# Kernel tuning notes

Measured on AMD Instinct MI355X. Metric: run time of the kernel, lower is better.

## Reference

```python
import jax, jax.numpy as jnp
import numpy as np

NEG_SLOPE = 0.2  # PyG GATConv default leaky_relu slope


def gat_conv(x, src, dst, n, W, a_src, a_dst, bias, concat):
    """PyG-style GATConv (add_self_loops already applied to src/dst)."""
    H, C = a_src.shape
    h = (x @ W).reshape(n, H, C)                      # [N,H,C]
    al_src = jnp.einsum('nhc,hc->nh', h, a_src)       # [N,H]
    al_dst = jnp.einsum('nhc,hc->nh', h, a_dst)       # [N,H]
    e = jax.nn.leaky_relu(al_src[src] + al_dst[dst], NEG_SLOPE)  # [E,H]
    # segment softmax over incoming edges of each dst node
    m = jax.ops.segment_max(e, dst, num_segments=n)   # [N,H]
    ex = jnp.exp(e - m[dst])
    denom = jax.ops.segment_sum(ex, dst, num_segments=n)
    alpha = ex / denom[dst]                            # [E,H]
    out = jax.ops.segment_sum(h[src] * alpha[:, :, None], dst, num_segments=n)  # [N,H,C]
    if concat:
        out = out.reshape(n, H * C)
    else:
        out = out.mean(axis=1)
    return out + bias


def setup_inputs() -> dict:
    key = jax.random.key(0)
    ks = jax.random.split(key, 12)
    N, E = 100000, 1600000
    IN, HID, OUT, H = 128, 16, 32, 4
    x = jax.random.normal(ks[0], (N, IN), dtype=jnp.float32)
    edge_index = jax.random.randint(ks[1], (2, E), 0, N, dtype=jnp.int64)
    s = 0.1
    W1 = jax.random.normal(ks[2], (IN, H * HID), dtype=jnp.float32) * s
    a_src1 = jax.random.normal(ks[3], (H, HID), dtype=jnp.float32) * s
    a_dst1 = jax.random.normal(ks[4], (H, HID), dtype=jnp.float32) * s
    b1 = jnp.zeros((H * HID,), dtype=jnp.float32)
    W2 = jax.random.normal(ks[5], (H * HID, H * OUT), dtype=jnp.float32) * s
    a_src2 = jax.random.normal(ks[6], (H, OUT), dtype=jnp.float32) * s
    a_dst2 = jax.random.normal(ks[7], (H, OUT), dtype=jnp.float32) * s
    b2 = jnp.zeros((OUT,), dtype=jnp.float32)
    return {"x": x, "edge_index": edge_index,
            "W1": W1, "a_src1": a_src1, "a_dst1": a_dst1, "b1": b1,
            "W2": W2, "a_src2": a_src2, "a_dst2": a_dst2, "b2": b2}


def reference(x, edge_index, W1, a_src1, a_dst1, b1, W2, a_src2, a_dst2, b2):
    n = x.shape[0]
    loop = jnp.arange(n, dtype=edge_index.dtype)
    src = jnp.concatenate([edge_index[0], loop])
    dst = jnp.concatenate([edge_index[1], loop])
    # dropout is identity at inference
    h = gat_conv(x, src, dst, n, W1, a_src1, a_dst1, b1, concat=True)
    h = gat_conv(h, src, dst, n, W2, a_src2, a_dst2, b2, concat=False)
    h = jax.nn.elu(h)
    return jax.nn.log_softmax(h, axis=1)
```

## Files before the change

kernel.cpp:

```cpp
#include <hip/hip_runtime.h>
#include <hip/hip_fp16.h>
#include <cstdint>
#include <cstddef>

#define NEG 0.2f
#define TILE 4096
#define WEXP(e) __expf((e) > 0.f ? (e) : NEG * (e))


__global__ __launch_bounds__(256) void bhist_k(const int* __restrict__ ei, int* __restrict__ bc, int E, int nbk) {
    __shared__ int sb[256];
    int t = threadIdx.x;
    sb[t] = 0;
    __syncthreads();
    int stride = gridDim.x * 256;
    for (int i = blockIdx.x * 256 + t; i < E; i += stride) {
        int d = __builtin_nontemporal_load(ei + E + i);
        atomicAdd(&sb[d >> 9], 1);
    }
    __syncthreads();
    if (t < nbk && sb[t] > 0) atomicAdd(&bc[t], sb[t]);
}


__global__ __launch_bounds__(256) void bscan_k(const int* __restrict__ bc, int* __restrict__ bb,
                                               int* __restrict__ curA, int nbk) {
    __shared__ int sm[256];
    int t = threadIdx.x;
    int v = (t < nbk) ? bc[t] : 0;
    sm[t] = v; __syncthreads();
    for (int off = 1; off < 256; off <<= 1) {
        int u = (t >= off) ? sm[t - off] : 0;
        __syncthreads();
        sm[t] += u;
        __syncthreads();
    }
    if (t < nbk) {
        int ex = sm[t] - v;
        bb[t] = ex;
        curA[t] = ex;
        if (t == nbk - 1) bb[nbk] = sm[t];
    }
}


__global__ __launch_bounds__(256) void partA_k(const int* __restrict__ ei, int* __restrict__ curA,
                                               uint2* __restrict__ pairs, int E, int nbk) {
    __shared__ int scnt[256];
    __shared__ int sc[256];
    __shared__ int sbase[256];
    __shared__ int gbase[256];
    __shared__ int cur2[256];
    __shared__ int ssrc[TILE];
    __shared__ int sdst[TILE];
    int t = threadIdx.x;
    int ntiles = (E + TILE - 1) / TILE;
    for (int tile = blockIdx.x; tile < ntiles; tile += gridDim.x) {
        int base = tile * TILE;
        int cntE = min(TILE, E - base);
        scnt[t] = 0;
        __syncthreads();
        int mys[16], myd[16];
        #pragma unroll
        for (int j = 0; j < 16; j++) {
            int i = base + t + 256 * j;
            int s = 0, d = -1;
            if (i < E) {
                s = __builtin_nontemporal_load(ei + i);
                d = __builtin_nontemporal_load(ei + E + i);
            }
            mys[j] = s; myd[j] = d;
            if (d >= 0) atomicAdd(&scnt[d >> 9], 1);
        }
        __syncthreads();
        sc[t] = scnt[t];
        __syncthreads();
        for (int off = 1; off < 256; off <<= 1) {
            int u = (t >= off) ? sc[t - off] : 0;
            __syncthreads();
            sc[t] += u;
            __syncthreads();
        }
        int myb = sc[t] - scnt[t];
        sbase[t] = myb;
        cur2[t] = myb;
        if (t < nbk && scnt[t] > 0) gbase[t] = atomicAdd(&curA[t], scnt[t]);
        __syncthreads();
        #pragma unroll
        for (int j = 0; j < 16; j++) {
            int d = myd[j];
            if (d >= 0) {
                int b = d >> 9;
                int pos = atomicAdd(&cur2[b], 1);
                ssrc[pos] = mys[j];
                sdst[pos] = d;
            }
        }
        __syncthreads();
        for (int i = t; i < cntE; i += 256) {
            int d = sdst[i];
            int b = d >> 9;
            int addr = gbase[b] + (i - sbase[b]);
            pairs[addr] = make_uint2((unsigned)ssrc[i], (unsigned)d);
        }
        __syncthreads();
    }
}


__global__ __launch_bounds__(256) void partB2_k(const uint2* __restrict__ pin, const int* __restrict__ bb,
                                                int* __restrict__ rp, int* __restrict__ cnt,
                                                int* __restrict__ srcout, int N) {
    __shared__ int cur[512];
    __shared__ int sc[512];
    int b = blockIdx.x, t = threadIdx.x;
    int d0 = b << 9;
    cur[t] = 0; cur[t + 256] = 0;
    __syncthreads();
    int ebase = bb[b], eend = bb[b + 1];
    for (int j = ebase + t; j < eend; j += 256) {
        int d = (int)pin[j].y;
        atomicAdd(&cur[d - d0], 1);
    }
    __syncthreads();
    sc[t] = cur[t]; sc[t + 256] = cur[t + 256];
    __syncthreads();
    for (int off = 1; off <= 256; off <<= 1) {
        int a0 = (t >= off) ? sc[t - off] : 0;
        int a1 = sc[t + 256 - off];
        __syncthreads();
        sc[t] += a0; sc[t + 256] += a1;
        __syncthreads();
    }
    int base0 = ebase + sc[t] - cur[t];
    int base1 = ebase + sc[t + 256] - cur[t + 256];
    if (d0 + t < N)       { rp[d0 + t] = base0;       cnt[d0 + t] = cur[t]; }
    if (d0 + t + 256 < N) { rp[d0 + t + 256] = base1; cnt[d0 + t + 256] = cur[t + 256]; }
    cur[t] = base0; cur[t + 256] = base1;
    __syncthreads();
    for (int j = ebase + t; j < eend; j += 256) {
        uint2 p = pin[j];
        int d = (int)p.y;
        int pos = atomicAdd(&cur[d - d0], 1);
        srcout[pos] = (int)p.x;
    }
}


__global__ __launch_bounds__(256) void gemm1_k(const float* __restrict__ x, const float* __restrict__ W,
                                               const float* __restrict__ a_src, const float* __restrict__ a_dst,
                                               __half* __restrict__ h, float* __restrict__ alsrc,
                                               float* __restrict__ aldst, int N) {
    __shared__ float Bs[128 * 64];
    __shared__ float xs[64][68];
    int t = threadIdx.x;
    for (int i = t; i < 128 * 64 / 4; i += 256)
        ((float4*)Bs)[i] = ((const float4*)W)[i];
    int ct = t & 15, rt = t >> 4;
    int head = ct >> 2, cq = ct & 3;
    float asv[4], adv[4];
    #pragma unroll
    for (int j = 0; j < 4; j++) {
        asv[j] = a_src[head * 16 + 4 * cq + j];
        adv[j] = a_dst[head * 16 + 4 * cq + j];
    }
    int ntiles = (N + 63) >> 6;
    for (int tile = blockIdx.x; tile < ntiles; tile += gridDim.x) {
        int r0 = tile << 6;
        float acc[4][4];
        #pragma unroll
        for (int i = 0; i < 4; i++)
            #pragma unroll
            for (int j = 0; j < 4; j++) acc[i][j] = 0.f;
        for (int kc = 0; kc < 128; kc += 64) {
            __syncthreads();
            int srow = t >> 4, sf4 = t & 15;
            #pragma unroll
            for (int p = 0; p < 4; p++) {
                int r = r0 + srow + 16 * p;
                float4 v = make_float4(0.f, 0.f, 0.f, 0.f);
                if (r < N) v = *(const float4*)(x + (size_t)r * 128 + kc + 4 * sf4);
                *(float4*)&xs[srow + 16 * p][4 * sf4] = v;
            }
            __syncthreads();
            #pragma unroll 4
            for (int k = 0; k < 64; k++) {
                float4 bv = *(float4*)&Bs[(kc + k) * 64 + 4 * ct];
                #pragma unroll
                for (int i = 0; i < 4; i++) {
                    float xv = xs[4 * rt + i][k];
                    acc[i][0] = fmaf(xv, bv.x, acc[i][0]);
                    acc[i][1] = fmaf(xv, bv.y, acc[i][1]);
                    acc[i][2] = fmaf(xv, bv.z, acc[i][2]);
                    acc[i][3] = fmaf(xv, bv.w, acc[i][3]);
                }
            }
        }
        #pragma unroll
        for (int i = 0; i < 4; i++) {
            int r = r0 + 4 * rt + i;
            float ps = 0.f, pd = 0.f;
            #pragma unroll
            for (int j = 0; j < 4; j++) {
                ps = fmaf(acc[i][j], asv[j], ps);
                pd = fmaf(acc[i][j], adv[j], pd);
            }
            ps += __shfl_xor(ps, 1); ps += __shfl_xor(ps, 2);
            pd += __shfl_xor(pd, 1); pd += __shfl_xor(pd, 2);
            if (r < N) {
                __half2 h0 = __floats2half2_rn(acc[i][0], acc[i][1]);
                __half2 h1 = __floats2half2_rn(acc[i][2], acc[i][3]);
                *(__half2*)(h + (size_t)r * 64 + 4 * ct) = h0;
                *(__half2*)(h + (size_t)r * 64 + 4 * ct + 2) = h1;
                if (cq == 0) { alsrc[r * 4 + head] = ps; aldst[r * 4 + head] = pd; }
            }
        }
    }
}


__global__ __launch_bounds__(256) void node1_k(const __half* __restrict__ h, const int* __restrict__ srccol,
                                               const float* __restrict__ alsrc, const float* __restrict__ aldst,
                                               const int* __restrict__ rp, const int* __restrict__ cnt,
                                               const float* __restrict__ bias, __half* __restrict__ out, int N) {
    int t = threadIdx.x;
    int d = (blockIdx.x * 256 + t) >> 4;
    if (d >= N) return;
    int c = t & 15;
    int hc = c >> 2;
    const __half2* hb = (const __half2*)h;
    unsigned co = 2u * c;
    float ad = aldst[d * 4 + hc];
    float e = alsrc[d * 4 + hc] + ad;
    float w = WEXP(e);
    float den = w;
    __half2 wp = __float2half2_rn(w);
    uint2 u = *(const uint2*)(hb + ((unsigned)d << 5) + co);
    __half2 acc0 = __hmul2(wp, *(__half2*)&u.x);
    __half2 acc1 = __hmul2(wp, *(__half2*)&u.y);
    int start = rp[d], deg = cnt[d];
    int i = 0;
    for (; i + 3 < deg; i += 4) {
        int s0 = srccol[start + i];
        int s1 = srccol[start + i + 1];
        int s2 = srccol[start + i + 2];
        int s3 = srccol[start + i + 3];
        uint2 u0 = *(const uint2*)(hb + ((unsigned)s0 << 5) + co);
        uint2 u1 = *(const uint2*)(hb + ((unsigned)s1 << 5) + co);
        uint2 u2 = *(const uint2*)(hb + ((unsigned)s2 << 5) + co);
        uint2 u3 = *(const uint2*)(hb + ((unsigned)s3 << 5) + co);
        float e0 = alsrc[s0 * 4 + hc] + ad;
        float e1 = alsrc[s1 * 4 + hc] + ad;
        float e2 = alsrc[s2 * 4 + hc] + ad;
        float e3 = alsrc[s3 * 4 + hc] + ad;
        float w0 = WEXP(e0);
        float w1 = WEXP(e1);
        float w2 = WEXP(e2);
        float w3 = WEXP(e3);
        den += (w0 + w1) + (w2 + w3);
        __half2 p0 = __float2half2_rn(w0), p1 = __float2half2_rn(w1);
        __half2 p2 = __float2half2_rn(w2), p3 = __float2half2_rn(w3);
        acc0 = __hfma2(p0, *(__half2*)&u0.x, acc0);
        acc1 = __hfma2(p0, *(__half2*)&u0.y, acc1);
        acc0 = __hfma2(p1, *(__half2*)&u1.x, acc0);
        acc1 = __hfma2(p1, *(__half2*)&u1.y, acc1);
        acc0 = __hfma2(p2, *(__half2*)&u2.x, acc0);
        acc1 = __hfma2(p2, *(__half2*)&u2.y, acc1);
        acc0 = __hfma2(p3, *(__half2*)&u3.x, acc0);
        acc1 = __hfma2(p3, *(__half2*)&u3.y, acc1);
    }
    for (; i < deg; i++) {
        int s = srccol[start + i];
        uint2 us = *(const uint2*)(hb + ((unsigned)s << 5) + co);
        float es = alsrc[s * 4 + hc] + ad;
        float ws = WEXP(es);
        den += ws;
        __half2 wps = __float2half2_rn(ws);
        acc0 = __hfma2(wps, *(__half2*)&us.x, acc0);
        acc1 = __hfma2(wps, *(__half2*)&us.y, acc1);
    }
    float inv = 1.f / den;
    float2 f0 = __half22float2(acc0), f1 = __half22float2(acc1);
    float4 b = *(const float4*)(bias + 4 * c);
    __half2 o0 = __floats2half2_rn(f0.x * inv + b.x, f0.y * inv + b.y);
    __half2 o1 = __floats2half2_rn(f1.x * inv + b.z, f1.y * inv + b.w);
    uint2 o; o.x = *(unsigned*)&o0; o.y = *(unsigned*)&o1;
    *(uint2*)(out + (size_t)d * 64 + 4 * c) = o;
}


__global__ __launch_bounds__(256) void prew_k(const float* __restrict__ W2, const float* __restrict__ as2,
                                              const float* __restrict__ ad2, float* __restrict__ was,
                                              float* __restrict__ wad) {
    int t = threadIdx.x;
    int k = t >> 2, hh = t & 3;
    const float* wrow = W2 + k * 128 + hh * 32;
    const float* av = as2 + hh * 32;
    const float* dv = ad2 + hh * 32;
    float s = 0.f, ds = 0.f;
    #pragma unroll 8
    for (int c = 0; c < 32; c++) {
        float w = wrow[c];
        s = fmaf(w, av[c], s);
        ds = fmaf(w, dv[c], ds);
    }
    was[t] = s;
    wad[t] = ds;
}


__global__ __launch_bounds__(256) void alv2_k(const __half* __restrict__ h1o, const float* __restrict__ was,
                                              const float* __restrict__ wad, float* __restrict__ alsrc,
                                              float* __restrict__ aldst, int N) {
    int t = threadIdx.x;
    int d = (blockIdx.x * 256 + t) >> 4;
    if (d >= N) return;
    int c = t & 15;
    uint2 u = *(const uint2*)(h1o + (size_t)d * 64 + 4 * c);
    float2 f0 = __half22float2(*(__half2*)&u.x);
    float2 f1 = __half22float2(*(__half2*)&u.y);
    float v0 = f0.x, v1 = f0.y, v2 = f1.x, v3 = f1.y;
    const float4* was4 = (const float4*)was;
    const float4* wad4 = (const float4*)wad;
    float4 wa0 = was4[4 * c + 0], wa1 = was4[4 * c + 1], wa2 = was4[4 * c + 2], wa3 = was4[4 * c + 3];
    float4 wd0 = wad4[4 * c + 0], wd1 = wad4[4 * c + 1], wd2 = wad4[4 * c + 2], wd3 = wad4[4 * c + 3];
    float4 ps, pd;
    ps.x = fmaf(v0, wa0.x, fmaf(v1, wa1.x, fmaf(v2, wa2.x, v3 * wa3.x)));
    ps.y = fmaf(v0, wa0.y, fmaf(v1, wa1.y, fmaf(v2, wa2.y, v3 * wa3.y)));
    ps.z = fmaf(v0, wa0.z, fmaf(v1, wa1.z, fmaf(v2, wa2.z, v3 * wa3.z)));
    ps.w = fmaf(v0, wa0.w, fmaf(v1, wa1.w, fmaf(v2, wa2.w, v3 * wa3.w)));
    pd.x = fmaf(v0, wd0.x, fmaf(v1, wd1.x, fmaf(v2, wd2.x, v3 * wd3.x)));
    pd.y = fmaf(v0, wd0.y, fmaf(v1, wd1.y, fmaf(v2, wd2.y, v3 * wd3.y)));
    pd.z = fmaf(v0, wd0.z, fmaf(v1, wd1.z, fmaf(v2, wd2.z, v3 * wd3.z)));
    pd.w = fmaf(v0, wd0.w, fmaf(v1, wd1.w, fmaf(v2, wd2.w, v3 * wd3.w)));
    #pragma unroll
    for (int off = 1; off <= 8; off <<= 1) {
        ps.x += __shfl_xor(ps.x, off); ps.y += __shfl_xor(ps.y, off);
        ps.z += __shfl_xor(ps.z, off); ps.w += __shfl_xor(ps.w, off);
        pd.x += __shfl_xor(pd.x, off); pd.y += __shfl_xor(pd.y, off);
        pd.z += __shfl_xor(pd.z, off); pd.w += __shfl_xor(pd.w, off);
    }
    if (c == 0) {
        *(float4*)(alsrc + (size_t)d * 4) = ps;
        *(float4*)(aldst + (size_t)d * 4) = pd;
    }
}


#define EDGE2(U, F) { \
    float wa = WEXP(F.x + ad4.x), wb = WEXP(F.y + ad4.y); \
    float wc = WEXP(F.z + ad4.z), wd = WEXP(F.w + ad4.w); \
    dnA += wa; dnB += wb; dnC += wc; dnD += wd; \
    __half2 l = *(__half2*)&U.x, hh = *(__half2*)&U.y; \
    __half2 qa = __float2half2_rn(wa), qb = __float2half2_rn(wb); \
    __half2 qc = __float2half2_rn(wc), qd = __float2half2_rn(wd); \
    aA0 = __hfma2(qa, l, aA0); aA1 = __hfma2(qa, hh, aA1); \
    aB0 = __hfma2(qb, l, aB0); aB1 = __hfma2(qb, hh, aB1); \
    aC0 = __hfma2(qc, l, aC0); aC1 = __hfma2(qc, hh, aC1); \
    aD0 = __hfma2(qd, l, aD0); aD1 = __hfma2(qd, hh, aD1); }

__global__ __launch_bounds__(256) void node2_k(const __half* __restrict__ h1o, const int* __restrict__ srccol,
                                               const float* __restrict__ alsrc, const float* __restrict__ aldst,
                                               const int* __restrict__ rp, const int* __restrict__ cnt,
                                               __half* __restrict__ y, int N) {
    int t = threadIdx.x;
    int d = (blockIdx.x * 256 + t) >> 4;
    if (d >= N) return;
    int c = t & 15;
    const uint2* hb = (const uint2*)h1o;
    float4 ad4 = *(const float4*)(aldst + 4 * (size_t)d);
    float4 e4  = *(const float4*)(alsrc + 4 * (size_t)d);
    float wA = WEXP(e4.x + ad4.x);
    float wB = WEXP(e4.y + ad4.y);
    float wC = WEXP(e4.z + ad4.z);
    float wD = WEXP(e4.w + ad4.w);
    float dnA = wA, dnB = wB, dnC = wC, dnD = wD;
    uint2 u = hb[((size_t)d << 4) + c];
    __half2 lo = *(__half2*)&u.x, hi = *(__half2*)&u.y;
    __half2 pA = __float2half2_rn(wA), pB = __float2half2_rn(wB);
    __half2 pC = __float2half2_rn(wC), pD = __float2half2_rn(wD);
    __half2 aA0 = __hmul2(pA, lo), aA1 = __hmul2(pA, hi);
    __half2 aB0 = __hmul2(pB, lo), aB1 = __hmul2(pB, hi);
    __half2 aC0 = __hmul2(pC, lo), aC1 = __hmul2(pC, hi);
    __half2 aD0 = __hmul2(pD, lo), aD1 = __hmul2(pD, hi);
    int start = rp[d], deg = cnt[d];
    int i = 0;
    for (; i + 3 < deg; i += 4) {
        int s0 = srccol[start + i];
        int s1 = srccol[start + i + 1];
        int s2 = srccol[start + i + 2];
        int s3 = srccol[start + i + 3];
        uint2 u0 = hb[((size_t)s0 << 4) + c];
        uint2 u1 = hb[((size_t)s1 << 4) + c];
        uint2 u2 = hb[((size_t)s2 << 4) + c];
        uint2 u3 = hb[((size_t)s3 << 4) + c];
        float4 f0 = *(const float4*)(alsrc + 4 * (size_t)s0);
        float4 f1 = *(const float4*)(alsrc + 4 * (size_t)s1);
        float4 f2 = *(const float4*)(alsrc + 4 * (size_t)s2);
        float4 f3 = *(const float4*)(alsrc + 4 * (size_t)s3);
        EDGE2(u0, f0)
        EDGE2(u1, f1)
        EDGE2(u2, f2)
        EDGE2(u3, f3)
    }
    for (; i < deg; i++) {
        int s = srccol[start + i];
        uint2 us = hb[((size_t)s << 4) + c];
        float4 fs = *(const float4*)(alsrc + 4 * (size_t)s);
        EDGE2(us, fs)
    }
    float ivA = 0.25f / dnA, ivB = 0.25f / dnB, ivC = 0.25f / dnC, ivD = 0.25f / dnD;
    __half2 jA = __float2half2_rn(ivA), jB = __float2half2_rn(ivB);
    __half2 jC = __float2half2_rn(ivC), jD = __float2half2_rn(ivD);
    uint2 oA, oB, oC, oD;
    ((__half2*)&oA)[0] = __hmul2(jA, aA0); ((__half2*)&oA)[1] = __hmul2(jA, aA1);
    ((__half2*)&oB)[0] = __hmul2(jB, aB0); ((__half2*)&oB)[1] = __hmul2(jB, aB1);
    ((__half2*)&oC)[0] = __hmul2(jC, aC0); ((__half2*)&oC)[1] = __hmul2(jC, aC1);
    ((__half2*)&oD)[0] = __hmul2(jD, aD0); ((__half2*)&oD)[1] = __hmul2(jD, aD1);
    __half* yp = y + (size_t)d * 256 + 4u * (unsigned)c;
    *(uint2*)(yp)       = oA;
    *(uint2*)(yp + 64)  = oB;
    *(uint2*)(yp + 128) = oC;
    *(uint2*)(yp + 192) = oD;
}


__global__ __launch_bounds__(256) void gemm3_k(const __half* __restrict__ y, const float* __restrict__ W2,
                                               const float* __restrict__ bias, float* __restrict__ out, int N) {
    __shared__ __half2 ws[256 * 16];
    __shared__ __half2 ys[64 * 134];
    int t = threadIdx.x;
    for (int i = t; i < 4096; i += 256) {
        int kp = i >> 4, c2 = i & 15;
        int hh = kp >> 6, kk = kp & 63;
        const float* wp = W2 + kk * 128 + hh * 32 + 2 * c2;
        ws[i] = __floats2half2_rn(wp[0], wp[1]);
    }
    int ct = t & 7, rt = t >> 3;
    float4 b4 = *(const float4*)(bias + 4 * ct);
    int ntiles = (N + 63) >> 6;
    for (int tile = blockIdx.x; tile < ntiles; tile += gridDim.x) {
        int r0 = tile << 6;
        __syncthreads();
        for (int i = t; i < 64 * 64; i += 256) {
            int row = i >> 6, k4 = i & 63;
            uint2 v = make_uint2(0u, 0u);
            int r = r0 + row;
            if (r < N) v = *(const uint2*)(y + (size_t)r * 256 + 4 * k4);
            *(uint2*)&ys[row * 134 + 2 * k4] = v;
        }
        __syncthreads();
        float acc[2][4];
        #pragma unroll
        for (int r = 0; r < 2; r++)
            #pragma unroll
            for (int j = 0; j < 4; j++) acc[r][j] = 0.f;
        const __half2* yr0 = ys + (2 * rt) * 134;
        const __half2* yr1 = ys + (2 * rt + 1) * 134;
        #pragma unroll 4
        for (int k2 = 0; k2 < 128; k2++) {
            const __half2* wk0 = ws + (2 * k2) * 16;
            const __half2* wk1 = wk0 + 16;
            float2 wA0 = __half22float2(wk0[2 * ct]);
            float2 wA1 = __half22float2(wk0[2 * ct + 1]);
            float2 wB0 = __half22float2(wk1[2 * ct]);
            float2 wB1 = __half22float2(wk1[2 * ct + 1]);
            float2 xa = __half22float2(yr0[k2]);
            float2 xb = __half22float2(yr1[k2]);
            acc[0][0] = fmaf(xa.x, wA0.x, acc[0][0]); acc[0][1] = fmaf(xa.x, wA0.y, acc[0][1]);
            acc[0][2] = fmaf(xa.x, wA1.x, acc[0][2]); acc[0][3] = fmaf(xa.x, wA1.y, acc[0][3]);
            acc[0][0] = fmaf(xa.y, wB0.x, acc[0][0]); acc[0][1] = fmaf(xa.y, wB0.y, acc[0][1]);
            acc[0][2] = fmaf(xa.y, wB1.x, acc[0][2]); acc[0][3] = fmaf(xa.y, wB1.y, acc[0][3]);
            acc[1][0] = fmaf(xb.x, wA0.x, acc[1][0]); acc[1][1] = fmaf(xb.x, wA0.y, acc[1][1]);
            acc[1][2] = fmaf(xb.x, wA1.x, acc[1][2]); acc[1][3] = fmaf(xb.x, wA1.y, acc[1][3]);
            acc[1][0] = fmaf(xb.y, wB0.x, acc[1][0]); acc[1][1] = fmaf(xb.y, wB0.y, acc[1][1]);
            acc[1][2] = fmaf(xb.y, wB1.x, acc[1][2]); acc[1][3] = fmaf(xb.y, wB1.y, acc[1][3]);
        }
        #pragma unroll
        for (int r = 0; r < 2; r++) {
            int row = r0 + 2 * rt + r;
            float ev0 = acc[r][0] + b4.x;
            float ev1 = acc[r][1] + b4.y;
            float ev2 = acc[r][2] + b4.z;
            float ev3 = acc[r][3] + b4.w;
            ev0 = ev0 > 0.f ? ev0 : __expf(ev0) - 1.f;
            ev1 = ev1 > 0.f ? ev1 : __expf(ev1) - 1.f;
            ev2 = ev2 > 0.f ? ev2 : __expf(ev2) - 1.f;
            ev3 = ev3 > 0.f ? ev3 : __expf(ev3) - 1.f;
            float mx = fmaxf(fmaxf(ev0, ev1), fmaxf(ev2, ev3));
            #pragma unroll
            for (int off = 1; off <= 4; off <<= 1) mx = fmaxf(mx, __shfl_xor(mx, off));
            float sm = __expf(ev0 - mx) + __expf(ev1 - mx) + __expf(ev2 - mx) + __expf(ev3 - mx);
            #pragma unroll
            for (int off = 1; off <= 4; off <<= 1) sm += __shfl_xor(sm, off);
            float ls = mx + __logf(sm);
            if (row < N) {
                float4 o;
                o.x = ev0 - ls; o.y = ev1 - ls; o.z = ev2 - ls; o.w = ev3 - ls;
                *(float4*)(out + (size_t)row * 32 + 4 * ct) = o;
            }
        }
    }
}


extern "C" void kernel_launch(void* const* d_in, const int* in_sizes, int n_in,
                              void* d_out, int out_size, void* d_ws, size_t ws_size,
                              hipStream_t stream) {
    const float* x   = (const float*)d_in[0];
    const int*   ei  = (const int*)d_in[1];
    const float* W1  = (const float*)d_in[2];
    const float* as1 = (const float*)d_in[3];
    const float* ad1 = (const float*)d_in[4];
    const float* b1  = (const float*)d_in[5];
    const float* W2  = (const float*)d_in[6];
    const float* as2 = (const float*)d_in[7];
    const float* ad2 = (const float*)d_in[8];
    const float* b2  = (const float*)d_in[9];
    float* out = (float*)d_out;
    int N = in_sizes[0] / 128;
    int E = in_sizes[1] / 2;

    char* base = (char*)d_ws;
    size_t off = 0;
    auto alloc = [&](size_t bytes) -> char* {
        char* p = base + off;
        off = (off + bytes + 255) & ~(size_t)255;
        return p;
    };
    __half* y     = (__half*)alloc((size_t)N * 256 * 2);
    __half* h1h   = (__half*)y;
    uint2*  pairs = (uint2*)((char*)y + (size_t)N * 64 * 2);
    __half* h1o   = (__half*)alloc((size_t)N * 64 * 2);
    float* alsrc1 = (float*)alloc((size_t)N * 4 * 4);
    float* aldst1 = (float*)alloc((size_t)N * 4 * 4);
    float* alsrc2 = (float*)alloc((size_t)N * 4 * 4);
    float* aldst2 = (float*)alloc((size_t)N * 4 * 4);
    float* was    = (float*)alloc(256 * 4);
    float* wad    = (float*)alloc(256 * 4);
    int* cnt  = (int*)alloc((size_t)N * 4);
    int* rp   = (int*)alloc((size_t)N * 4);
    int* curA = (int*)alloc(256 * 4);
    int* bc   = (int*)alloc(256 * 4);
    int* bb   = (int*)alloc(260 * 4);
    int* srccol = (int*)alloc((size_t)E * 4);

    int nbk = (N + 511) >> 9;
    int ntilesA = (E + TILE - 1) / TILE;

    prew_k<<<1, 256, 0, stream>>>(W2, as2, ad2, was, wad);
    hipMemsetAsync(bc, 0, 256 * 4, stream);
    bhist_k<<<512, 256, 0, stream>>>(ei, bc, E, nbk);
    bscan_k<<<1, 256, 0, stream>>>(bc, bb, curA, nbk);
    partA_k<<<ntilesA, 256, 0, stream>>>(ei, curA, pairs, E, nbk);
    partB2_k<<<nbk, 256, 0, stream>>>(pairs, bb, rp, cnt, srccol, N);

    gemm1_k<<<768, 256, 0, stream>>>(x, W1, as1, ad1, h1h, alsrc1, aldst1, N);
    node1_k<<<(N + 15) / 16, 256, 0, stream>>>(h1h, srccol, alsrc1, aldst1, rp, cnt, b1, h1o, N);
    alv2_k<<<(N + 15) / 16, 256, 0, stream>>>(h1o, was, wad, alsrc2, aldst2, N);
    node2_k<<<(N + 15) / 16, 256, 0, stream>>>(h1o, srccol, alsrc2, aldst2, rp, cnt, y, N);
    gemm3_k<<<768, 256, 0, stream>>>(y, W2, b2, out, N);
}
```

Measured before the change: 351.3 us.

## Distribute edge weight computation across lanes in node2 and use fdot2 in gemm3

In node2_k each of the 16 lanes now computes one head's attention weight for one of four edges and shares it with the other lanes by shuffle. This replaces four redundant float4 alsrc loads and exps per lane. gemm3_k uses packed-half dot2 instructions with a re-laid-out weight tile, and launches one block per 64-row tile instead of a persistent grid. gemm1's grid size also changes. The shuffle approach adds cross-lane traffic, and the grid changes alter occupancy and how often weights are reloaded per block.

```diff
diff --git a/kernel.cpp b/kernel.cpp
--- a/kernel.cpp
+++ b/kernel.cpp
@@ -6,6 +6,19 @@
 #define NEG 0.2f
 #define TILE 4096
 #define WEXP(e) __expf((e) > 0.f ? (e) : NEG * (e))
+
+typedef _Float16 fh2 __attribute__((ext_vector_type(2)));
+
+__device__ __forceinline__ fh2 bfh2(unsigned v) { fh2 r; *(unsigned*)&r = v; return r; }
+__device__ __forceinline__ __half2 bch(int v) { __half2 r; *(int*)&r = v; return r; }
+
+#if __has_builtin(__builtin_amdgcn_fdot2)
+#define FDOT2(a, b, c) __builtin_amdgcn_fdot2((a), (b), (c), false)
+#else
+__device__ __forceinline__ float FDOT2(fh2 a, fh2 b, float c) {
+    return fmaf((float)a.x, (float)b.x, fmaf((float)a.y, (float)b.y, c));
+}
+#endif
 
 
 __global__ __launch_bounds__(256) void bhist_k(const int* __restrict__ ei, int* __restrict__ bc, int E, int nbk) {
@@ -347,17 +360,16 @@
 }
 
 
-#define EDGE2(U, F) { \
-    float wa = WEXP(F.x + ad4.x), wb = WEXP(F.y + ad4.y); \
-    float wc = WEXP(F.z + ad4.z), wd = WEXP(F.w + ad4.w); \
-    dnA += wa; dnB += wb; dnC += wc; dnD += wd; \
-    __half2 l = *(__half2*)&U.x, hh = *(__half2*)&U.y; \
-    __half2 qa = __float2half2_rn(wa), qb = __float2half2_rn(wb); \
-    __half2 qc = __float2half2_rn(wc), qd = __float2half2_rn(wd); \
-    aA0 = __hfma2(qa, l, aA0); aA1 = __hfma2(qa, hh, aA1); \
-    aB0 = __hfma2(qb, l, aB0); aB1 = __hfma2(qb, hh, aB1); \
-    aC0 = __hfma2(qc, l, aC0); aC1 = __hfma2(qc, hh, aC1); \
-    aD0 = __hfma2(qd, l, aD0); aD1 = __hfma2(qd, hh, aD1); }
+#define EDGE_SH(J, U) { \
+    __half2 l_ = *(__half2*)&U.x, h_ = *(__half2*)&U.y; \
+    __half2 qa = bch(__shfl(wi, 4 * J + 0, 16)); \
+    __half2 qb = bch(__shfl(wi, 4 * J + 1, 16)); \
+    __half2 qc = bch(__shfl(wi, 4 * J + 2, 16)); \
+    __half2 qd = bch(__shfl(wi, 4 * J + 3, 16)); \
+    aA0 = __hfma2(qa, l_, aA0); aA1 = __hfma2(qa, h_, aA1); \
+    aB0 = __hfma2(qb, l_, aB0); aB1 = __hfma2(qb, h_, aB1); \
+    aC0 = __hfma2(qc, l_, aC0); aC1 = __hfma2(qc, h_, aC1); \
+    aD0 = __hfma2(qd, l_, aD0); aD1 = __hfma2(qd, h_, aD1); }
 
 __global__ __launch_bounds__(256) void node2_k(const __half* __restrict__ h1o, const int* __restrict__ srccol,
                                                const float* __restrict__ alsrc, const float* __restrict__ aldst,
@@ -367,22 +379,24 @@
     int d = (blockIdx.x * 256 + t) >> 4;
     if (d >= N) return;
     int c = t & 15;
+    int eh = c >> 2;
+    int hh = c & 3;
     const uint2* hb = (const uint2*)h1o;
-    float4 ad4 = *(const float4*)(aldst + 4 * (size_t)d);
-    float4 e4  = *(const float4*)(alsrc + 4 * (size_t)d);
-    float wA = WEXP(e4.x + ad4.x);
-    float wB = WEXP(e4.y + ad4.y);
-    float wC = WEXP(e4.z + ad4.z);
-    float wD = WEXP(e4.w + ad4.w);
-    float dnA = wA, dnB = wB, dnC = wC, dnD = wD;
+    float myad = aldst[d * 4 + hh];
+    float selfw = WEXP(alsrc[d * 4 + hh] + myad);
+    __half2 selfh = __float2half2_rn(selfw);
+    int selfi = *(int*)&selfh;
+    float mden = (eh == 0) ? selfw : 0.f;
     uint2 u = hb[((size_t)d << 4) + c];
     __half2 lo = *(__half2*)&u.x, hi = *(__half2*)&u.y;
-    __half2 pA = __float2half2_rn(wA), pB = __float2half2_rn(wB);
-    __half2 pC = __float2half2_rn(wC), pD = __float2half2_rn(wD);
-    __half2 aA0 = __hmul2(pA, lo), aA1 = __hmul2(pA, hi);
-    __half2 aB0 = __hmul2(pB, lo), aB1 = __hmul2(pB, hi);
-    __half2 aC0 = __hmul2(pC, lo), aC1 = __hmul2(pC, hi);
-    __half2 aD0 = __hmul2(pD, lo), aD1 = __hmul2(pD, hi);
+    __half2 sA = bch(__shfl(selfi, 0, 16));
+    __half2 sB = bch(__shfl(selfi, 1, 16));
+    __half2 sC = bch(__shfl(selfi, 2, 16));
+    __half2 sD = bch(__shfl(selfi, 3, 16));
+    __half2 aA0 = __hmul2(sA, lo), aA1 = __hmul2(sA, hi);
+    __half2 aB0 = __hmul2(sB, lo), aB1 = __hmul2(sB, hi);
+    __half2 aC0 = __hmul2(sC, lo), aC1 = __hmul2(sC, hi);
+    __half2 aD0 = __hmul2(sD, lo), aD1 = __hmul2(sD, hi);
     int start = rp[d], deg = cnt[d];
     int i = 0;
     for (; i + 3 < deg; i += 4) {
@@ -394,24 +408,33 @@
         uint2 u1 = hb[((size_t)s1 << 4) + c];
         uint2 u2 = hb[((size_t)s2 << 4) + c];
         uint2 u3 = hb[((size_t)s3 << 4) + c];
-        float4 f0 = *(const float4*)(alsrc + 4 * (size_t)s0);
-        float4 f1 = *(const float4*)(alsrc + 4 * (size_t)s1);
-        float4 f2 = *(const float4*)(alsrc + 4 * (size_t)s2);
-        float4 f3 = *(const float4*)(alsrc + 4 * (size_t)s3);
-        EDGE2(u0, f0)
-        EDGE2(u1, f1)
-        EDGE2(u2, f2)
-        EDGE2(u3, f3)
+        int my = (eh == 0) ? s0 : (eh == 1) ? s1 : (eh == 2) ? s2 : s3;
+        float w = WEXP(alsrc[my * 4 + hh] + myad);
+        mden += w;
+        __half2 wh = __float2half2_rn(w);
+        int wi = *(int*)&wh;
+        EDGE_SH(0, u0)
+        EDGE_SH(1, u1)
+        EDGE_SH(2, u2)
+        EDGE_SH(3, u3)
     }
     for (; i < deg; i++) {
         int s = srccol[start + i];
         uint2 us = hb[((size_t)s << 4) + c];
-        float4 fs = *(const float4*)(alsrc + 4 * (size_t)s);
-        EDGE2(us, fs)
-    }
-    float ivA = 0.25f / dnA, ivB = 0.25f / dnB, ivC = 0.25f / dnC, ivD = 0.25f / dnD;
-    __half2 jA = __float2half2_rn(ivA), jB = __float2half2_rn(ivB);
-    __half2 jC = __float2half2_rn(ivC), jD = __float2half2_rn(ivD);
+        float w = WEXP(alsrc[s * 4 + hh] + myad);
+        mden += (eh == 0) ? w : 0.f;
+        __half2 wh = __float2half2_rn(w);
+        int wi = *(int*)&wh;
+        EDGE_SH(0, us)
+    }
+    mden += __shfl_xor(mden, 4, 16);
+    mden += __shfl_xor(mden, 8, 16);
+    float dnA = __shfl(mden, 0, 16);
+    float dnB = __shfl(mden, 1, 16);
+    float dnC = __shfl(mden, 2, 16);
+    float dnD = __shfl(mden, 3, 16);
+    __half2 jA = __float2half2_rn(0.25f / dnA), jB = __float2half2_rn(0.25f / dnB);
+    __half2 jC = __float2half2_rn(0.25f / dnC), jD = __float2half2_rn(0.25f / dnD);
     uint2 oA, oB, oC, oD;
     ((__half2*)&oA)[0] = __hmul2(jA, aA0); ((__half2*)&oA)[1] = __hmul2(jA, aA1);
     ((__half2*)&oB)[0] = __hmul2(jB, aB0); ((__half2*)&oB)[1] = __hmul2(jB, aB1);
@@ -427,78 +450,74 @@
 
 __global__ __launch_bounds__(256) void gemm3_k(const __half* __restrict__ y, const float* __restrict__ W2,
                                                const float* __restrict__ bias, float* __restrict__ out, int N) {
-    __shared__ __half2 ws[256 * 16];
-    __shared__ __half2 ys[64 * 134];
+    __shared__ unsigned wk[128 * 32];
+    __shared__ unsigned ys[64 * 130];
     int t = threadIdx.x;
     for (int i = t; i < 4096; i += 256) {
-        int kp = i >> 4, c2 = i & 15;
-        int hh = kp >> 6, kk = kp & 63;
-        const float* wp = W2 + kk * 128 + hh * 32 + 2 * c2;
-        ws[i] = __floats2half2_rn(wp[0], wp[1]);
+        int k2 = i >> 5, col = i & 31;
+        int hh = k2 >> 5, kk = (2 * k2) & 63;
+        float f0 = W2[kk * 128 + hh * 32 + col];
+        float f1 = W2[(kk + 1) * 128 + hh * 32 + col];
+        __half2 hv = __floats2half2_rn(f0, f1);
+        wk[i] = *(unsigned*)&hv;
     }
     int ct = t & 7, rt = t >> 3;
     float4 b4 = *(const float4*)(bias + 4 * ct);
-    int ntiles = (N + 63) >> 6;
-    for (int tile = blockIdx.x; tile < ntiles; tile += gridDim.x) {
-        int r0 = tile << 6;
-        __syncthreads();
-        for (int i = t; i < 64 * 64; i += 256) {
-            int row = i >> 6, k4 = i & 63;
-            uint2 v = make_uint2(0u, 0u);
-            int r = r0 + row;
-            if (r < N) v = *(const uint2*)(y + (size_t)r * 256 + 4 * k4);
-            *(uint2*)&ys[row * 134 + 2 * k4] = v;
-        }
-        __syncthreads();
-        float acc[2][4];
-        #pragma unroll
-        for (int r = 0; r < 2; r++)
-            #pragma unroll
-            for (int j = 0; j < 4; j++) acc[r][j] = 0.f;
-        const __half2* yr0 = ys + (2 * rt) * 134;
-        const __half2* yr1 = ys + (2 * rt + 1) * 134;
-        #pragma unroll 4
-        for (int k2 = 0; k2 < 128; k2++) {
-            const __half2* wk0 = ws + (2 * k2) * 16;
-            const __half2* wk1 = wk0 + 16;
-            float2 wA0 = __half22float2(wk0[2 * ct]);
-            float2 wA1 = __half22float2(wk0[2 * ct + 1]);
-            float2 wB0 = __half22float2(wk1[2 * ct]);
-            float2 wB1 = __half22float2(wk1[2 * ct + 1]);
-            float2 xa = __half22float2(yr0[k2]);
-            float2 xb = __half22float2(yr1[k2]);
-            acc[0][0] = fmaf(xa.x, wA0.x, acc[0][0]); acc[0][1] = fmaf(xa.x, wA0.y, acc[0][1]);
-            acc[0][2] = fmaf(xa.x, wA1.x, acc[0][2]); acc[0][3] = fmaf(xa.x, wA1.y, acc[0][3]);
-            acc[0][0] = fmaf(xa.y, wB0.x, acc[0][0]); acc[0][1] = fmaf(xa.y, wB0.y, acc[0][1]);
-            acc[0][2] = fmaf(xa.y, wB1.x, acc[0][2]); acc[0][3] = fmaf(xa.y, wB1.y, acc[0][3]);
-            acc[1][0] = fmaf(xb.x, wA0.x, acc[1][0]); acc[1][1] = fmaf(xb.x, wA0.y, acc[1][1]);
-            acc[1][2] = fmaf(xb.x, wA1.x, acc[1][2]); acc[1][3] = fmaf(xb.x, wA1.y, acc[1][3]);
-            acc[1][0] = fmaf(xb.y, wB0.x, acc[1][0]); acc[1][1] = fmaf(xb.y, wB0.y, acc[1][1]);
-            acc[1][2] = fmaf(xb.y, wB1.x, acc[1][2]); acc[1][3] = fmaf(xb.y, wB1.y, acc[1][3]);
-        }
-        #pragma unroll
-        for (int r = 0; r < 2; r++) {
-            int row = r0 + 2 * rt + r;
-            float ev0 = acc[r][0] + b4.x;
-            float ev1 = acc[r][1] + b4.y;
-            float ev2 = acc[r][2] + b4.z;
-            float ev3 = acc[r][3] + b4.w;
-            ev0 = ev0 > 0.f ? ev0 : __expf(ev0) - 1.f;
-            ev1 = ev1 > 0.f ? ev1 : __expf(ev1) - 1.f;
-            ev2 = ev2 > 0.f ? ev2 : __expf(ev2) - 1.f;
-            ev3 = ev3 > 0.f ? ev3 : __expf(ev3) - 1.f;
-            float mx = fmaxf(fmaxf(ev0, ev1), fmaxf(ev2, ev3));
-            #pragma unroll
-            for (int off = 1; off <= 4; off <<= 1) mx = fmaxf(mx, __shfl_xor(mx, off));
-            float sm = __expf(ev0 - mx) + __expf(ev1 - mx) + __expf(ev2 - mx) + __expf(ev3 - mx);
-            #pragma unroll
-            for (int off = 1; off <= 4; off <<= 1) sm += __shfl_xor(sm, off);
-            float ls = mx + __logf(sm);
-            if (row < N) {
-                float4 o;
-                o.x = ev0 - ls; o.y = ev1 - ls; o.z = ev2 - ls; o.w = ev3 - ls;
-                *(float4*)(out + (size_t)row * 32 + 4 * ct) = o;
-            }
+    int r0 = blockIdx.x << 6;
+    for (int i = t; i < 64 * 64; i += 256) {
+        int row = i >> 6, k4 = i & 63;
+        uint2 v = make_uint2(0u, 0u);
+        int r = r0 + row;
+        if (r < N) v = *(const uint2*)(y + (size_t)r * 256 + 4 * k4);
+        *(uint2*)&ys[row * 130 + 2 * k4] = v;
+    }
+    __syncthreads();
+    float acc[2][4];
+    #pragma unroll
+    for (int r = 0; r < 2; r++)
+        #pragma unroll
+        for (int j = 0; j < 4; j++) acc[r][j] = 0.f;
+    const unsigned* yr0 = ys + (2 * rt) * 130;
+    const unsigned* yr1 = yr0 + 130;
+    const unsigned* wp = wk + 4 * ct;
+    #pragma unroll 8
+    for (int k2 = 0; k2 < 128; k2++) {
+        fh2 xa = bfh2(yr0[k2]);
+        fh2 xb = bfh2(yr1[k2]);
+        uint2 w01 = *(const uint2*)&wp[k2 * 32];
+        uint2 w23 = *(const uint2*)&wp[k2 * 32 + 2];
+        fh2 w0 = bfh2(w01.x), w1 = bfh2(w01.y), w2 = bfh2(w23.x), w3 = bfh2(w23.y);
+        acc[0][0] = FDOT2(xa, w0, acc[0][0]);
+        acc[0][1] = FDOT2(xa, w1, acc[0][1]);
+        acc[0][2] = FDOT2(xa, w2, acc[0][2]);
+        acc[0][3] = FDOT2(xa, w3, acc[0][3]);
+        acc[1][0] = FDOT2(xb, w0, acc[1][0]);
+        acc[1][1] = FDOT2(xb, w1, acc[1][1]);
+        acc[1][2] = FDOT2(xb, w2, acc[1][2]);
+        acc[1][3] = FDOT2(xb, w3, acc[1][3]);
+    }
+    #pragma unroll
+    for (int r = 0; r < 2; r++) {
+        int row = r0 + 2 * rt + r;
+        float ev0 = acc[r][0] + b4.x;
+        float ev1 = acc[r][1] + b4.y;
+        float ev2 = acc[r][2] + b4.z;
+        float ev3 = acc[r][3] + b4.w;
+        ev0 = ev0 > 0.f ? ev0 : __expf(ev0) - 1.f;
+        ev1 = ev1 > 0.f ? ev1 : __expf(ev1) - 1.f;
+        ev2 = ev2 > 0.f ? ev2 : __expf(ev2) - 1.f;
+        ev3 = ev3 > 0.f ? ev3 : __expf(ev3) - 1.f;
+        float mx = fmaxf(fmaxf(ev0, ev1), fmaxf(ev2, ev3));
+        #pragma unroll
+        for (int off = 1; off <= 4; off <<= 1) mx = fmaxf(mx, __shfl_xor(mx, off));
+        float sm = __expf(ev0 - mx) + __expf(ev1 - mx) + __expf(ev2 - mx) + __expf(ev3 - mx);
+        #pragma unroll
+        for (int off = 1; off <= 4; off <<= 1) sm += __shfl_xor(sm, off);
+        float ls = mx + __logf(sm);
+        if (row < N) {
+            float4 o;
+            o.x = ev0 - ls; o.y = ev1 - ls; o.z = ev2 - ls; o.w = ev3 - ls;
+            *(float4*)(out + (size_t)row * 32 + 4 * ct) = o;
         }
     }
 }
@@ -547,6 +566,7 @@
 
     int nbk = (N + 511) >> 9;
     int ntilesA = (E + TILE - 1) / TILE;
+    int nt1 = (N + 63) >> 6;
 
     prew_k<<<1, 256, 0, stream>>>(W2, as2, ad2, was, wad);
     hipMemsetAsync(bc, 0, 256 * 4, stream);
@@ -555,9 +575,9 @@
     partA_k<<<ntilesA, 256, 0, stream>>>(ei, curA, pairs, E, nbk);
     partB2_k<<<nbk, 256, 0, stream>>>(pairs, bb, rp, cnt, srccol, N);
 
-    gemm1_k<<<768, 256, 0, stream>>>(x, W1, as1, ad1, h1h, alsrc1, aldst1, N);
+    gemm1_k<<<(nt1 + 1) / 2, 256, 0, stream>>>(x, W1, as1, ad1, h1h, alsrc1, aldst1, N);
     node1_k<<<(N + 15) / 16, 256, 0, stream>>>(h1h, srccol, alsrc1, aldst1, rp, cnt, b1, h1o, N);
     alv2_k<<<(N + 15) / 16, 256, 0, stream>>>(h1o, was, wad, alsrc2, aldst2, N);
     node2_k<<<(N + 15) / 16, 256, 0, stream>>>(h1o, srccol, alsrc2, aldst2, rp, cnt, y, N);
-    gemm3_k<<<768, 256, 0, stream>>>(y, W2, b2, out, N);
-}
+    gemm3_k<<<nt1, 256, 0, stream>>>(y, W2, b2, out, N);
+}
```

Measured after the change: 344.0 us. -2.1%, faster.
